# Optimization experiments

Measured on AMD Instinct MI355X. Metric: run time of the kernel, lower is better.

The kernel has to match this reference:

```python
import jax, jax.numpy as jnp
import numpy as np
import math

IMG_CHL = 1024
L_CHL = 512
N_PTS = 4096  # pinned by nn.LayerNorm(4096)
H = 256
W = 256
HEADS = 4
VOXEL = 1.0 / 256.0
PC_MIN = 0.0
BEV_STRIDE = 1.0
LN_EPS = 1e-5


def setup_inputs() -> dict:
    key = jax.random.key(0)
    ks = jax.random.split(key, 6)
    point_features = jax.random.normal(ks[0], (1, L_CHL, N_PTS), jnp.float32)
    kp = jax.random.uniform(ks[1], (N_PTS, 4), dtype=jnp.float32)
    keypoints = kp.at[:, 0].set(0.0)  # batch index column = 0 (batch_size=1)
    bev_features = jax.random.normal(ks[2], (1, IMG_CHL, H, W), jnp.float32)
    conv_L_w = jax.random.normal(ks[3], (L_CHL, L_CHL), jnp.float32) * 0.02
    conv_L_b = jnp.zeros((L_CHL,), jnp.float32)
    img_head_w = jax.random.normal(ks[4], (HEADS, L_CHL, IMG_CHL), jnp.float32) * 0.02
    img_head_b = jnp.zeros((HEADS, L_CHL), jnp.float32)
    ln_w = jnp.ones((N_PTS,), jnp.float32)
    ln_b = jnp.zeros((N_PTS,), jnp.float32)
    conv_fusion_w = jax.random.normal(ks[5], (L_CHL, L_CHL), jnp.float32) * 0.02
    conv_fusion_b = jnp.zeros((L_CHL,), jnp.float32)
    return {
        "point_features": point_features,
        "keypoints": keypoints,
        "bev_features": bev_features,
        "conv_L_w": conv_L_w,
        "conv_L_b": conv_L_b,
        "img_head_w": img_head_w,
        "img_head_b": img_head_b,
        "ln_w": ln_w,
        "ln_b": ln_b,
        "conv_fusion_w": conv_fusion_w,
        "conv_fusion_b": conv_fusion_b,
    }


def _bilinear_interpolate(im, x, y):
    """im: (H, W, C); x, y: (N,). Mirrors bilinear_interpolate_torch (clamped corners)."""
    x0 = jnp.clip(jnp.floor(x).astype(jnp.int32), 0, im.shape[1] - 1)
    x1 = jnp.clip(jnp.floor(x).astype(jnp.int32) + 1, 0, im.shape[1] - 1)
    y0 = jnp.clip(jnp.floor(y).astype(jnp.int32), 0, im.shape[0] - 1)
    y1 = jnp.clip(jnp.floor(y).astype(jnp.int32) + 1, 0, im.shape[0] - 1)
    Ia = im[y0, x0]  # (N, C)
    Ib = im[y1, x0]
    Ic = im[y0, x1]
    Id = im[y1, x1]
    x0f, x1f = x0.astype(x.dtype), x1.astype(x.dtype)
    y0f, y1f = y0.astype(y.dtype), y1.astype(y.dtype)
    wa = (x1f - x) * (y1f - y)
    wb = (x1f - x) * (y - y0f)
    wc = (x - x0f) * (y1f - y)
    wd = (x - x0f) * (y - y0f)
    return Ia * wa[:, None] + Ib * wb[:, None] + Ic * wc[:, None] + Id * wd[:, None]


def reference(point_features, keypoints, bev_features, conv_L_w, conv_L_b,
              img_head_w, img_head_b, ln_w, ln_b, conv_fusion_w, conv_fusion_b):
    # --- interpolate_from_bev_features (batch_size=1, all keypoints in batch 0) ---
    x_idxs = (keypoints[:, 1] - PC_MIN) / VOXEL / BEV_STRIDE
    y_idxs = (keypoints[:, 2] - PC_MIN) / VOXEL / BEV_STRIDE
    im = jnp.transpose(bev_features[0], (1, 2, 0))  # (H, W, C)
    point_bev = _bilinear_interpolate(im, x_idxs, y_idxs)  # (N, IMG_CHL)
    img_features = point_bev.T[None]  # (1, IMG_CHL, N)

    # --- Fusion_Conv_att ---
    # 1x1 Conv1d == channel matmul
    L_query = jnp.einsum('oc,bcn->bon', conv_L_w, point_features) + conv_L_b[None, :, None]  # (1, L, N)
    keys = jnp.einsum('hoc,bcn->hbon', img_head_w, img_features) + img_head_b[:, None, :, None]  # (4, 1, L, N)
    dk = L_CHL
    score = jnp.sum(keys * L_query[None], axis=2)[:, 0, :] / math.sqrt(dk)  # (4, N)
    weightmap = jax.nn.softmax(score, axis=0)[None]  # (1, 4, N) softmax over heads
    z = jnp.einsum('hn,hln->ln', weightmap[0], keys[:, 0])[None]  # (1, L, N)

    t = z + L_query
    mu = jnp.mean(t, axis=-1, keepdims=True)
    var = jnp.mean((t - mu) ** 2, axis=-1, keepdims=True)
    t = (t - mu) / jnp.sqrt(var + LN_EPS) * ln_w + ln_b  # LayerNorm over the 4096 point axis

    fusion_features = jnp.einsum('oc,bcn->bon', conv_fusion_w, t) + conv_fusion_b[None, :, None]
    return fusion_features, weightmap
```

## Files before the change

### kernel.cpp

```cpp
#include <hip/hip_runtime.h>

typedef unsigned short u16;
typedef unsigned int   u32;

typedef short s16x8 __attribute__((ext_vector_type(8)));
typedef float f32x4 __attribute__((ext_vector_type(4)));

__device__ __forceinline__ float b2f(u16 u) {
    u32 x = ((u32)u) << 16;
    float f;
    __builtin_memcpy(&f, &x, 4);
    return f;
}

__device__ __forceinline__ u16 f2b(float f) {
    u32 x;
    __builtin_memcpy(&x, &f, 4);
    u32 r = (x + 0x7fffu + ((x >> 16) & 1u)) >> 16;
    return (u16)r;
}

__global__ void prep_points(const float* __restrict__ kp,
                            int4* __restrict__ pts_off,
                            float4* __restrict__ pts_w,
                            int* __restrict__ perm) {
    __shared__ int cnt[256];
    __shared__ int base[256];
    const int t = threadIdx.x;
    cnt[t] = 0;
    __syncthreads();
    int buck[16];
    #pragma unroll
    for (int j = 0; j < 16; j++) {
        const int n = j * 256 + t;
        const float x = kp[n * 4 + 1] * 256.0f;
        const float y = kp[n * 4 + 2] * 256.0f;
        const int x0 = min(max((int)floorf(x), 0), 255);
        const int y0 = min(max((int)floorf(y), 0), 255);
        const int b = (y0 >> 3) * 8 + (x0 >> 5);
        buck[j] = b;
        atomicAdd(&cnt[b], 1);
    }
    __syncthreads();
    if (t < 64) {
        int a0 = cnt[t * 4], a1 = cnt[t * 4 + 1], a2 = cnt[t * 4 + 2], a3 = cnt[t * 4 + 3];
        int tot = a0 + a1 + a2 + a3;
        int pre = tot;
        #pragma unroll
        for (int off = 1; off < 64; off <<= 1) {
            int v = __shfl_up(pre, off);
            if (t >= off) pre += v;
        }
        int excl = pre - tot;
        base[t * 4]     = excl;
        base[t * 4 + 1] = excl + a0;
        base[t * 4 + 2] = excl + a0 + a1;
        base[t * 4 + 3] = excl + a0 + a1 + a2;
    }
    __syncthreads();
    cnt[t] = 0;
    __syncthreads();
    #pragma unroll
    for (int j = 0; j < 16; j++) {
        const int n = j * 256 + t;
        const float x = kp[n * 4 + 1] * 256.0f;
        const float y = kp[n * 4 + 2] * 256.0f;
        const float xf = floorf(x), yf = floorf(y);
        const int x0 = min(max((int)xf, 0), 255);
        const int x1 = min(max((int)xf + 1, 0), 255);
        const int y0 = min(max((int)yf, 0), 255);
        const int y1 = min(max((int)yf + 1, 0), 255);
        const float x0f = (float)x0, x1f = (float)x1;
        const float y0f = (float)y0, y1f = (float)y1;
        float4 w;
        w.x = (x1f - x) * (y1f - y);
        w.y = (x1f - x) * (y - y0f);
        w.z = (x - x0f) * (y1f - y);
        w.w = (x - x0f) * (y - y0f);
        int4 o;
        o.x = y0 * 256 + x0;
        o.y = y1 * 256 + x0;
        o.z = y0 * 256 + x1;
        o.w = y1 * 256 + x1;
        const int b = buck[j];
        const int pos = base[b] + atomicAdd(&cnt[b], 1);
        perm[pos] = n;
        pts_off[pos] = o;
        pts_w[pos] = w;
    }
}

__global__ __launch_bounds__(256) void interp_sorted(const float* __restrict__ bev,
                                                     const int4* __restrict__ pts_off,
                                                     const float4* __restrict__ pts_w,
                                                     u16* __restrict__ img) {
    const int c = blockIdx.x;
    const float* plane = bev + (size_t)c * 65536;
    const int base_i = blockIdx.y * 1024;
    const int t = threadIdx.x;
    #pragma unroll
    for (int j = 0; j < 4; j++) {
        const int i = base_i + j * 256 + t;
        const int4 o = pts_off[i];
        const float4 w = pts_w[i];
        const float v = plane[o.x] * w.x + plane[o.y] * w.y +
                        plane[o.z] * w.z + plane[o.w] * w.w;
        img[(size_t)c * 4096 + i] = f2b(v);
    }
}

__global__ void convert_params(const float* clw, const float* ihw, const float* cfw,
                               const float* clb, const float* ihb,
                               const float* lnw, const float* lnb, const float* cfb,
                               u16* __restrict__ canon) {
    const int total = 2632704;
    for (int i = blockIdx.x * 256 + threadIdx.x; i < total; i += gridDim.x * 256) {
        const float* src; int off;
        if (i < 262144)       { src = clw; off = i; }
        else if (i < 2359296) { src = ihw; off = i - 262144; }
        else if (i < 2621440) { src = cfw; off = i - 2359296; }
        else if (i < 2621952) { src = clb; off = i - 2621440; }
        else if (i < 2624000) { src = ihb; off = i - 2621952; }
        else if (i < 2628096) { src = lnw; off = i - 2624000; }
        else if (i < 2632192) { src = lnb; off = i - 2628096; }
        else                  { src = cfb; off = i - 2632192; }
        canon[i] = f2b(src[off]);
    }
}

template <int ISF>
__global__ void transpose_any(const void* __restrict__ in, u16* __restrict__ out,
                              int R, int C, const int* __restrict__ perm) {
    __shared__ u16 tile[64][65];
    const int t = threadIdx.x;
    const int r0 = blockIdx.y * 64, c0 = blockIdx.x * 64;
    #pragma unroll
    for (int i = 0; i < 16; i++) {
        int idx = i * 256 + t;
        int r = idx >> 6, c = idx & 63;
        tile[r][c] = ISF ? f2b(((const float*)in)[(size_t)(r0 + r) * C + c0 + c])
                         : ((const u16*)in)[(size_t)(r0 + r) * C + c0 + c];
    }
    __syncthreads();
    #pragma unroll
    for (int i = 0; i < 16; i++) {
        int idx = i * 256 + t;
        int c = idx >> 6, r = idx & 63;
        int row = perm ? perm[c0 + c] : (c0 + c);
        out[(size_t)row * R + r0 + r] = tile[r][c];
    }
}

template <int OB>
__global__ __launch_bounds__(256) void gemm_bt(const u16* __restrict__ A,
                                               const u16* __restrict__ BT,
                                               const u16* __restrict__ bias,
                                               void* __restrict__ Cout,
                                               int M, int N, int K) {
    __shared__ __align__(16) u16 As[128 * 40];
    __shared__ __align__(16) u16 Bs[128 * 40];
    const int tid = threadIdx.x;
    const int lane = tid & 63;
    const int w = tid >> 6;
    const int m0 = blockIdx.y * 128;
    const int n0 = blockIdx.x * 128;
    const int wm = (w >> 1) * 64;
    const int wn = (w & 1) * 64;

    f32x4 acc[4][4] = {};

    for (int k0 = 0; k0 < K; k0 += 32) {
        __syncthreads();
        #pragma unroll
        for (int i = 0; i < 2; i++) {
            int s = i * 256 + tid;
            int row = s >> 2, kc = s & 3;
            *(uint4*)&As[row * 40 + kc * 8] =
                *(const uint4*)&A[(size_t)(m0 + row) * K + k0 + kc * 8];
            *(uint4*)&Bs[row * 40 + kc * 8] =
                *(const uint4*)&BT[(size_t)(n0 + row) * K + k0 + kc * 8];
        }
        __syncthreads();

        const int q = lane >> 4, r = lane & 15;
        s16x8 af[4], bfr[4];
        #pragma unroll
        for (int mt = 0; mt < 4; mt++)
            af[mt] = *(const s16x8*)&As[(wm + mt * 16 + r) * 40 + q * 8];
        #pragma unroll
        for (int nt = 0; nt < 4; nt++)
            bfr[nt] = *(const s16x8*)&Bs[(wn + nt * 16 + r) * 40 + q * 8];
        #pragma unroll
        for (int mt = 0; mt < 4; mt++)
            #pragma unroll
            for (int nt = 0; nt < 4; nt++)
                acc[mt][nt] = __builtin_amdgcn_mfma_f32_16x16x32_bf16(
                    af[mt], bfr[nt], acc[mt][nt], 0, 0, 0);
    }

    const int q = lane >> 4, cn = lane & 15;
    #pragma unroll
    for (int mt = 0; mt < 4; mt++) {
        #pragma unroll
        for (int i = 0; i < 4; i++) {
            int gm = m0 + wm + mt * 16 + q * 4 + i;
            float bv = b2f(bias[gm]);
            #pragma unroll
            for (int nt = 0; nt < 4; nt++) {
                int gn = n0 + wn + nt * 16 + cn;
                float v = acc[mt][nt][i] + bv;
                if (OB)
                    ((u16*)Cout)[(size_t)gm * N + gn] = f2b(v);
                else
                    ((float*)Cout)[(size_t)gm * N + gn] = v;
            }
        }
    }
}

__global__ void score_partial(const u16* __restrict__ keys,
                              const float* __restrict__ lq,
                              float* __restrict__ spart) {
    __shared__ float red[4][4][64];
    const int nl = threadIdx.x & 63;
    const int ls = threadIdx.x >> 6;
    const int n = blockIdx.x * 64 + nl;
    const int lbase = blockIdx.y * 128 + ls * 32;
    float acc[4] = {0.f, 0.f, 0.f, 0.f};
    for (int i = 0; i < 32; i++) {
        const int l = lbase + i;
        const float qv = lq[l * 4096 + n];
        #pragma unroll
        for (int h = 0; h < 4; h++)
            acc[h] += b2f(keys[(size_t)(h * 512 + l) * 4096 + n]) * qv;
    }
    #pragma unroll
    for (int h = 0; h < 4; h++) red[h][ls][nl] = acc[h];
    __syncthreads();
    if (threadIdx.x < 64) {
        #pragma unroll
        for (int h = 0; h < 4; h++) {
            float s = red[h][0][nl] + red[h][1][nl] + red[h][2][nl] + red[h][3][nl];
            spart[(size_t)(blockIdx.y * 4 + h) * 4096 + n] = s;
        }
    }
}

__global__ void score_finalize(const float* __restrict__ spart,
                               float* __restrict__ wm_ws,
                               float* __restrict__ out) {
    const int n = blockIdx.x * 256 + threadIdx.x;
    const float scale = 0.044194173824159216f;
    float s[4];
    #pragma unroll
    for (int h = 0; h < 4; h++) {
        float v = 0.f;
        #pragma unroll
        for (int lc = 0; lc < 4; lc++) v += spart[(size_t)(lc * 4 + h) * 4096 + n];
        s[h] = v * scale;
    }
    float mx = fmaxf(fmaxf(s[0], s[1]), fmaxf(s[2], s[3]));
    float e[4], sum = 0.f;
    #pragma unroll
    for (int h = 0; h < 4; h++) { e[h] = expf(s[h] - mx); sum += e[h]; }
    const float inv = 1.0f / sum;
    #pragma unroll
    for (int h = 0; h < 4; h++) {
        float wv = e[h] * inv;
        wm_ws[h * 4096 + n] = wv;
        out[2097152 + (size_t)h * 4096 + n] = wv;
    }
}

__global__ __launch_bounds__(256) void compute_t_ln(const u16* __restrict__ keys,
                                                    const float* __restrict__ lq,
                                                    const float* __restrict__ wm_ws,
                                                    const float* __restrict__ lnw,
                                                    const float* __restrict__ lnb,
                                                    u16* __restrict__ tnorm) {
    const int l = blockIdx.x;
    const int t = threadIdx.x;
    float tv[16];
    float s = 0.f, ss = 0.f;
    #pragma unroll
    for (int j = 0; j < 16; j++) {
        const int n = j * 256 + t;
        float v = lq[l * 4096 + n];
        #pragma unroll
        for (int h = 0; h < 4; h++)
            v += wm_ws[h * 4096 + n] * b2f(keys[(size_t)(h * 512 + l) * 4096 + n]);
        tv[j] = v;
        s += v;
        ss += v * v;
    }
    for (int off = 32; off > 0; off >>= 1) {
        s += __shfl_down(s, off);
        ss += __shfl_down(ss, off);
    }
    __shared__ float bs[4], bss[4];
    const int w = t >> 6, lane = t & 63;
    if (lane == 0) { bs[w] = s; bss[w] = ss; }
    __syncthreads();
    const float S = bs[0] + bs[1] + bs[2] + bs[3];
    const float SS = bss[0] + bss[1] + bss[2] + bss[3];
    const float mu = S * (1.0f / 4096.0f);
    const float rstd = rsqrtf(SS * (1.0f / 4096.0f) - mu * mu + 1e-5f);
    #pragma unroll
    for (int j = 0; j < 16; j++) {
        const int n = j * 256 + t;
        const float v = (tv[j] - mu) * rstd * lnw[n] + lnb[n];
        tnorm[(size_t)l * 4096 + n] = f2b(v);
    }
}

extern "C" void kernel_launch(void* const* d_in, const int* in_sizes, int n_in,
                              void* d_out, int out_size, void* d_ws, size_t ws_size,
                              hipStream_t stream) {
    const float* pf  = (const float*)d_in[0];
    const float* kp  = (const float*)d_in[1];
    const float* bev = (const float*)d_in[2];
    const float* clw = (const float*)d_in[3];
    const float* clb = (const float*)d_in[4];
    const float* ihw = (const float*)d_in[5];
    const float* ihb = (const float*)d_in[6];
    const float* lnw = (const float*)d_in[7];
    const float* lnb = (const float*)d_in[8];
    const float* cfw = (const float*)d_in[9];
    const float* cfb = (const float*)d_in[10];
    float* out = (float*)d_out;

    char* ws = (char*)d_ws;
    u16*    img     = (u16*)(ws + 0);
    u16*    tnorm   = (u16*)(ws + 0);
    u16*    imgT    = (u16*)(ws + (8ull << 20));
    float*  lq      = (float*)(ws + (8ull << 20));
    u16*    keys    = (u16*)(ws + (16ull << 20));
    u16*    pfT     = (u16*)(ws + (32ull << 20));
    u16*    tT      = (u16*)(ws + (32ull << 20));
    float*  spart   = (float*)(ws + (36ull << 20));
    float*  wm_ws   = (float*)(ws + (36ull << 20) + 262144);
    u16*    canon   = (u16*)  (ws + (36ull << 20) + 332864);
    int4*   pts_off = (int4*) (ws + (42ull << 20));
    float4* pts_w   = (float4*)(ws + (42ull << 20) + 65536);
    int*    perm    = (int*)  (ws + (42ull << 20) + 131072);

    u16* clw_c = canon;
    u16* ihw_c = canon + 262144;
    u16* cfw_c = canon + 2359296;
    u16* clb_c = canon + 2621440;
    u16* ihb_c = canon + 2621952;
    u16* cfb_c = canon + 2632192;

    prep_points<<<1, 256, 0, stream>>>(kp, pts_off, pts_w, perm);
    convert_params<<<1024, 256, 0, stream>>>(clw, ihw, cfw, clb, ihb, lnw, lnb, cfb, canon);
    interp_sorted<<<dim3(1024, 4), 256, 0, stream>>>(bev, pts_off, pts_w, img);
    transpose_any<0><<<dim3(64, 16), 256, 0, stream>>>(img, imgT, 1024, 4096, perm);
    transpose_any<1><<<dim3(64, 8), 256, 0, stream>>>(pf, pfT, 512, 4096, nullptr);
    gemm_bt<1><<<dim3(32, 16), 256, 0, stream>>>(ihw_c, imgT, ihb_c, keys, 2048, 4096, 1024);
    gemm_bt<0><<<dim3(32, 4), 256, 0, stream>>>(clw_c, pfT, clb_c, lq, 512, 4096, 512);
    score_partial<<<dim3(64, 4), 256, 0, stream>>>(keys, lq, spart);
    score_finalize<<<16, 256, 0, stream>>>(spart, wm_ws, out);
    compute_t_ln<<<512, 256, 0, stream>>>(keys, lq, wm_ws, lnw, lnb, tnorm);
    transpose_any<0><<<dim3(64, 8), 256, 0, stream>>>(tnorm, tT, 512, 4096, nullptr);
    gemm_bt<0><<<dim3(32, 4), 256, 0, stream>>>(cfw_c, tT, cfb_c, out, 512, 4096, 512);
}
```

Baseline: 512.8 us.

## Use direct global-to-LDS loads in GEMM and shrink M tile for small GEMMs

Replaces the register-staged global-to-shared copies in the bf16 MFMA GEMM with global_load_lds direct-to-LDS loads, removing the row padding so the layout matches the 16-byte-per-lane write pattern. Adds a BM template parameter and uses 64-row tiles for the two 512x4096 GEMMs, doubling their block count to better fill the CUs. Also unrolls the score_partial inner loop. Dropping the padding can bring back LDS bank conflicts on the fragment reads, and the kernel still has no double buffering.

```diff
diff --git a/kernel.cpp b/kernel.cpp
--- a/kernel.cpp
+++ b/kernel.cpp
@@ -18,6 +18,12 @@
     __builtin_memcpy(&x, &f, 4);
     u32 r = (x + 0x7fffu + ((x >> 16) & 1u)) >> 16;
     return (u16)r;
+}
+
+__device__ __forceinline__ void gload_lds16(const u16* g, u16* l) {
+    __builtin_amdgcn_global_load_lds(
+        (const __attribute__((address_space(1))) void*)g,
+        (__attribute__((address_space(3))) void*)l, 16, 0, 0);
 }
 
 __global__ void prep_points(const float* __restrict__ kp,
@@ -151,56 +157,59 @@
     }
 }
 
-template <int OB>
+template <int BM, int OB>
 __global__ __launch_bounds__(256) void gemm_bt(const u16* __restrict__ A,
                                                const u16* __restrict__ BT,
                                                const u16* __restrict__ bias,
                                                void* __restrict__ Cout,
                                                int M, int N, int K) {
-    __shared__ __align__(16) u16 As[128 * 40];
-    __shared__ __align__(16) u16 Bs[128 * 40];
+    constexpr int MT = BM / 32;
+    __shared__ __align__(16) u16 As[BM * 32];
+    __shared__ __align__(16) u16 Bs[128 * 32];
     const int tid = threadIdx.x;
     const int lane = tid & 63;
     const int w = tid >> 6;
-    const int m0 = blockIdx.y * 128;
+    const int m0 = blockIdx.y * BM;
     const int n0 = blockIdx.x * 128;
-    const int wm = (w >> 1) * 64;
+    const int wm = (w >> 1) * (BM / 2);
     const int wn = (w & 1) * 64;
 
-    f32x4 acc[4][4] = {};
+    f32x4 acc[MT][4] = {};
+
+    const int q = lane >> 4, r = lane & 15;
 
     for (int k0 = 0; k0 < K; k0 += 32) {
         __syncthreads();
         #pragma unroll
+        for (int i = 0; i < BM / 64; i++) {
+            int s = i * 256 + tid;
+            gload_lds16(&A[(size_t)(m0 + (s >> 2)) * K + k0 + (s & 3) * 8], &As[s * 8]);
+        }
+        #pragma unroll
         for (int i = 0; i < 2; i++) {
             int s = i * 256 + tid;
-            int row = s >> 2, kc = s & 3;
-            *(uint4*)&As[row * 40 + kc * 8] =
-                *(const uint4*)&A[(size_t)(m0 + row) * K + k0 + kc * 8];
-            *(uint4*)&Bs[row * 40 + kc * 8] =
-                *(const uint4*)&BT[(size_t)(n0 + row) * K + k0 + kc * 8];
+            gload_lds16(&BT[(size_t)(n0 + (s >> 2)) * K + k0 + (s & 3) * 8], &Bs[s * 8]);
         }
         __syncthreads();
 
-        const int q = lane >> 4, r = lane & 15;
-        s16x8 af[4], bfr[4];
-        #pragma unroll
-        for (int mt = 0; mt < 4; mt++)
-            af[mt] = *(const s16x8*)&As[(wm + mt * 16 + r) * 40 + q * 8];
+        s16x8 af[MT], bfr[4];
+        #pragma unroll
+        for (int mt = 0; mt < MT; mt++)
+            af[mt] = *(const s16x8*)&As[(wm + mt * 16 + r) * 32 + q * 8];
         #pragma unroll
         for (int nt = 0; nt < 4; nt++)
-            bfr[nt] = *(const s16x8*)&Bs[(wn + nt * 16 + r) * 40 + q * 8];
-        #pragma unroll
-        for (int mt = 0; mt < 4; mt++)
+            bfr[nt] = *(const s16x8*)&Bs[(wn + nt * 16 + r) * 32 + q * 8];
+        #pragma unroll
+        for (int mt = 0; mt < MT; mt++)
             #pragma unroll
             for (int nt = 0; nt < 4; nt++)
                 acc[mt][nt] = __builtin_amdgcn_mfma_f32_16x16x32_bf16(
                     af[mt], bfr[nt], acc[mt][nt], 0, 0, 0);
     }
 
-    const int q = lane >> 4, cn = lane & 15;
-    #pragma unroll
-    for (int mt = 0; mt < 4; mt++) {
+    const int cn = lane & 15;
+    #pragma unroll
+    for (int mt = 0; mt < MT; mt++) {
         #pragma unroll
         for (int i = 0; i < 4; i++) {
             int gm = m0 + wm + mt * 16 + q * 4 + i;
@@ -227,6 +236,7 @@
     const int n = blockIdx.x * 64 + nl;
     const int lbase = blockIdx.y * 128 + ls * 32;
     float acc[4] = {0.f, 0.f, 0.f, 0.f};
+    #pragma unroll 8
     for (int i = 0; i < 32; i++) {
         const int l = lbase + i;
         const float qv = lq[l * 4096 + n];
@@ -356,11 +366,11 @@
     interp_sorted<<<dim3(1024, 4), 256, 0, stream>>>(bev, pts_off, pts_w, img);
     transpose_any<0><<<dim3(64, 16), 256, 0, stream>>>(img, imgT, 1024, 4096, perm);
     transpose_any<1><<<dim3(64, 8), 256, 0, stream>>>(pf, pfT, 512, 4096, nullptr);
-    gemm_bt<1><<<dim3(32, 16), 256, 0, stream>>>(ihw_c, imgT, ihb_c, keys, 2048, 4096, 1024);
-    gemm_bt<0><<<dim3(32, 4), 256, 0, stream>>>(clw_c, pfT, clb_c, lq, 512, 4096, 512);
+    gemm_bt<128, 1><<<dim3(32, 16), 256, 0, stream>>>(ihw_c, imgT, ihb_c, keys, 2048, 4096, 1024);
+    gemm_bt<64, 0><<<dim3(32, 8), 256, 0, stream>>>(clw_c, pfT, clb_c, lq, 512, 4096, 512);
     score_partial<<<dim3(64, 4), 256, 0, stream>>>(keys, lq, spart);
     score_finalize<<<16, 256, 0, stream>>>(spart, wm_ws, out);
     compute_t_ln<<<512, 256, 0, stream>>>(keys, lq, wm_ws, lnw, lnb, tnorm);
     transpose_any<0><<<dim3(64, 8), 256, 0, stream>>>(tnorm, tT, 512, 4096, nullptr);
-    gemm_bt<0><<<dim3(32, 4), 256, 0, stream>>>(cfw_c, tT, cfb_c, out, 512, 4096, 512);
-}
+    gemm_bt<64, 0><<<dim3(32, 8), 256, 0, stream>>>(cfw_c, tT, cfb_c, out, 512, 4096, 512);
+}
```

After: 518.0 us. No clear change (+1.0%).
